# Kernel optimization log

Measured on AMD Instinct MI355X. Metric: run time of the kernel, lower is better.

The kernel has to match this reference:

```python
import jax, jax.numpy as jnp
from jax import lax
import numpy as np

B, T, IN, H = 512, 2048, 6, 32


def _gru_dir(x, Wih, bih, Whh, bhh, reverse):
    # x: [B, T, in]; PyTorch GRU gate order: r, z, n
    xp = jnp.einsum('bti,gi->btg', x, Wih) + bih  # [B, T, 3H] precompute input GEMM
    h0 = jnp.zeros((x.shape[0], Whh.shape[1]), x.dtype)

    def step(h, xt):
        gh = h @ Whh.T + bhh                      # [B, 3H]
        xr, xz, xn = jnp.split(xt, 3, axis=-1)
        hr, hz, hn = jnp.split(gh, 3, axis=-1)
        r = jax.nn.sigmoid(xr + hr)
        z = jax.nn.sigmoid(xz + hz)
        n = jnp.tanh(xn + r * hn)
        h_new = (1.0 - z) * n + z * h
        return h_new, h_new

    xs = jnp.swapaxes(xp, 0, 1)                   # [T, B, 3H]
    _, hs = lax.scan(step, h0, xs, reverse=reverse)  # ys aligned to time index
    return jnp.swapaxes(hs, 0, 1)                 # [B, T, H]


def setup_inputs() -> dict:
    key = jax.random.key(0)
    ks = jax.random.split(key, 32)
    s = 1.0 / np.sqrt(H)
    u = lambda k, shp: jax.random.uniform(k, shp, jnp.float32, -s, s)
    inp = {'x': jax.random.normal(ks[0], (B, T, IN), jnp.float32)}
    i = 1
    for l, din in ((0, IN), (1, 2 * H)):
        for d in ('f', 'b'):
            inp[f'Wih_l{l}_{d}'] = u(ks[i], (3 * H, din)); i += 1
            inp[f'Whh_l{l}_{d}'] = u(ks[i], (3 * H, H)); i += 1
            inp[f'bih_l{l}_{d}'] = u(ks[i], (3 * H,)); i += 1
            inp[f'bhh_l{l}_{d}'] = u(ks[i], (3 * H,)); i += 1
    inp['fc1_w'] = u(ks[i], (16, 2 * H)); i += 1
    inp['fc1_b'] = u(ks[i], (16,)); i += 1
    inp['fc2_w'] = u(ks[i], (1, 16)); i += 1
    inp['fc2_b'] = u(ks[i], (1,))
    return inp


def reference(x, Wih_l0_f, Whh_l0_f, bih_l0_f, bhh_l0_f,
              Wih_l0_b, Whh_l0_b, bih_l0_b, bhh_l0_b,
              Wih_l1_f, Whh_l1_f, bih_l1_f, bhh_l1_f,
              Wih_l1_b, Whh_l1_b, bih_l1_b, bhh_l1_b,
              fc1_w, fc1_b, fc2_w, fc2_b):
    # layer 0 bidirectional
    f0 = _gru_dir(x, Wih_l0_f, bih_l0_f, Whh_l0_f, bhh_l0_f, reverse=False)
    b0 = _gru_dir(x, Wih_l0_b, bih_l0_b, Whh_l0_b, bhh_l0_b, reverse=True)
    h0 = jnp.concatenate([f0, b0], axis=-1)       # [B, T, 2H]; inter-layer dropout: eval mode -> identity
    # layer 1 bidirectional
    f1 = _gru_dir(h0, Wih_l1_f, bih_l1_f, Whh_l1_f, bhh_l1_f, reverse=False)
    b1 = _gru_dir(h0, Wih_l1_b, bih_l1_b, Whh_l1_b, bhh_l1_b, reverse=True)
    out = jnp.concatenate([f1, b1], axis=-1)      # [B, T, 2H]
    pooled = jnp.mean(out, axis=1)                # [B, 2H]
    h = jax.nn.relu(pooled @ fc1_w.T + fc1_b)     # dropout: eval mode -> identity
    return h @ fc2_w.T + fc2_b                    # [B, 1]
```

## Files before the change

kernel.cpp:

```cpp
#include <hip/hip_runtime.h>

#define TB  512
#define TT  2048
#define HID 32

typedef _Float16 f16;
typedef float f32x2 __attribute__((ext_vector_type(2)));


#define PKFMA(ACC, A, B) \
  asm("v_pk_fma_f32 %0, %1, %2, %0" : "+v"(ACC) : "v"(A), "v"(B))

__device__ __forceinline__ float half_swap(float x, int half){
#if __has_builtin(__builtin_amdgcn_permlane32_swap)
  typedef unsigned uv2 __attribute__((ext_vector_type(2)));
  uv2 r = __builtin_amdgcn_permlane32_swap(__float_as_uint(x), __float_as_uint(x),
                                           false, false);
  return __uint_as_float(half ? r.x : r.y);
#else
  (void)half;
  return __shfl_xor(x, 32, 64);
#endif
}

__global__ __launch_bounds__(64,1)
void gru_l0(const float* __restrict__ x,
            const float* __restrict__ Wih_f, const float* __restrict__ Whh_f,
            const float* __restrict__ bih_f, const float* __restrict__ bhh_f,
            const float* __restrict__ Wih_b, const float* __restrict__ Whh_b,
            const float* __restrict__ bih_b, const float* __restrict__ bhh_b,
            f16* __restrict__ h0)
{
  const int job  = blockIdx.x;
  const int b    = job >> 1;
  const int dir  = job & 1;
  const int lane = threadIdx.x;
  const int j    = lane & 31;
  const int half = lane >> 5;

  const float* Wih = dir ? Wih_b : Wih_f;
  const float* Whh = dir ? Whh_b : Whh_f;
  const float* bih = dir ? bih_b : bih_f;
  const float* bhh = dir ? bhh_b : bhh_f;

  const int mrow = half * 32 + j;
  const int nrow = 64 + j;

  f32x2 wh_m2[16], wh_n2[16];
  f32x2 wi_m2[3],  wi_n2[3];
  {
    const float4* wm4 = (const float4*)(Whh + mrow*32);
#pragma unroll
    for (int q=0;q<8;q++){ float4 v=wm4[q];
      wh_m2[2*q]   = f32x2{v.x, v.y};
      wh_m2[2*q+1] = f32x2{v.z, v.w}; }
    const float4* wn4 = (const float4*)(Whh + nrow*32);
#pragma unroll
    for (int q=0;q<8;q++){ float4 v=wn4[q];
      wh_n2[2*q]   = f32x2{v.x, v.y};
      wh_n2[2*q+1] = f32x2{v.z, v.w}; }
#pragma unroll
    for (int i=0;i<3;i++){
      wi_m2[i] = f32x2{Wih[mrow*6+2*i], Wih[mrow*6+2*i+1]};
      wi_n2[i] = f32x2{Wih[nrow*6+2*i], Wih[nrow*6+2*i+1]};
    }
  }
  const float b_m   = bih[mrow] + bhh[mrow];
  const float b_ihn = bih[nrow];
  const float b_hhn = bhh[nrow];

  __shared__ __align__(16) float hlds[32];

  double hj = 0.;

  const long t0    = dir ? (TT-1) : 0;
  const long tstep = dir ? -1 : 1;
  const float* xrow = x + ((size_t)b*TT + t0)*6;
  const long  xinc = tstep*6;
  f16* hout = h0 + ((size_t)b*TT + t0)*64 + dir*32;
  const long hinc = tstep*64;

  f32x2 hp[16];
#pragma unroll
  for (int k=0;k<16;k++) hp[k]=f32x2{0.f,0.f};

#define L0_STEP(XV)                                                          \
  {                                                                          \
    f32x2 SX2 = f32x2{0.f,0.f}, SN2 = f32x2{0.f,0.f};                        \
    PKFMA(SX2, wi_m2[0], XV[0]); PKFMA(SN2, wi_n2[0], XV[0]);                \
    PKFMA(SX2, wi_m2[1], XV[1]); PKFMA(SN2, wi_n2[1], XV[1]);                \
    PKFMA(SX2, wi_m2[2], XV[2]); PKFMA(SN2, wi_n2[2], XV[2]);                \
    float sx  = SX2.x + SX2.y;                                               \
    float sxn = SN2.x + SN2.y;                                               \
    f32x2 A0=f32x2{0.f,0.f}, A1=f32x2{0.f,0.f};                              \
    f32x2 C0=f32x2{0.f,0.f}, C1=f32x2{0.f,0.f};                              \
    _Pragma("unroll")                                                        \
    for (int k=0;k<8;k++){                                                   \
      PKFMA(A0, wh_m2[2*k],   hp[2*k]);                                      \
      PKFMA(A1, wh_m2[2*k+1], hp[2*k+1]);                                    \
      PKFMA(C0, wh_n2[2*k],   hp[2*k]);                                      \
      PKFMA(C1, wh_n2[2*k+1], hp[2*k+1]);                                    \
    }                                                                        \
    float hm   = (A0.x+A0.y)+(A1.x+A1.y);                                    \
    float sn_h = (C0.x+C0.y)+(C1.x+C1.y);                                    \
    float vf   = hm + sx + b_m;                                              \
    float varg = half ? -vf : vf;                                            \
    float ef   = __builtin_amdgcn_exp2f(varg * -1.44269504088896341f);       \
    float gmf  = __builtin_amdgcn_rcpf(1.f + ef);                            \
    float wf   = half_swap(gmf, half);                                       \
    float xn = sxn + b_ihn;                                                  \
    float hn = sn_h + b_hhn;                                                 \
    float af = fmaf(gmf, hn, xn);                                            \
    float e2 = __builtin_amdgcn_exp2f(af * 2.88539008177792682f);            \
    float nnf= 1.f - 2.f*__builtin_amdgcn_rcpf(1.f + e2);                    \
    double hnew = fma((double)wf, (double)nnf - hj, hj);                     \
    hj = hnew;                                                               \
    if (lane < 32){ hlds[j] = (float)hnew; hout[j] = (f16)hnew; }            \
    hout += hinc;                                                            \
    {                                                                        \
      const float4* h4 = (const float4*)hlds;                                \
      _Pragma("unroll")                                                      \
      for (int q=0;q<8;q++){ float4 v=h4[q];                                 \
        hp[2*q]   = f32x2{v.x, v.y};                                         \
        hp[2*q+1] = f32x2{v.z, v.w}; }                                       \
    }                                                                        \
  }

  f32x2 xa[3], xb[3];
  {
    const float2* p=(const float2*)xrow;
    xa[0]=f32x2{p[0].x,p[0].y}; xa[1]=f32x2{p[1].x,p[1].y}; xa[2]=f32x2{p[2].x,p[2].y};
    const float2* q=(const float2*)(xrow + xinc);
    xb[0]=f32x2{q[0].x,q[0].y}; xb[1]=f32x2{q[1].x,q[1].y}; xb[2]=f32x2{q[2].x,q[2].y};
  }
  const float* xld = xrow + 2*xinc;

#pragma unroll 1
  for (int it=0; it<TT; it+=2){
    L0_STEP(xa)
    if (it+2 < TT){
      const float2* p=(const float2*)xld;
      xa[0]=f32x2{p[0].x,p[0].y}; xa[1]=f32x2{p[1].x,p[1].y}; xa[2]=f32x2{p[2].x,p[2].y};
      xld += xinc;
    }
    L0_STEP(xb)
    if (it+3 < TT){
      const float2* p=(const float2*)xld;
      xb[0]=f32x2{p[0].x,p[0].y}; xb[1]=f32x2{p[1].x,p[1].y}; xb[2]=f32x2{p[2].x,p[2].y};
      xld += xinc;
    }
  }
#undef L0_STEP
}

__global__ __launch_bounds__(128,2)
void gru_l1(const f16* __restrict__ h0,
            const float* __restrict__ Wih_f, const float* __restrict__ Whh_f,
            const float* __restrict__ bih_f, const float* __restrict__ bhh_f,
            const float* __restrict__ Wih_b, const float* __restrict__ Whh_b,
            const float* __restrict__ bih_b, const float* __restrict__ bhh_b,
            float* __restrict__ pooled)
{
  const int job  = blockIdx.x;
  const int b    = job >> 1;
  const int dir  = job & 1;
  const int tid  = threadIdx.x;
  const int wid  = tid >> 6;
  const int lane = tid & 63;
  const int j    = lane & 31;
  const int half = lane >> 5;

  const float* Wih = dir ? Wih_b : Wih_f;
  const float* Whh = dir ? Whh_b : Whh_f;
  const float* bih = dir ? bih_b : bih_f;
  const float* bhh = dir ? bhh_b : bhh_f;

  const int mrow = half * 32 + j;
  const int nrow = 64 + j;

  __shared__ __align__(16) float hlds[32];
  __shared__ __align__(16) float ring[8*64];
  __shared__ __align__(16) float fx[8][64];
  __shared__ __align__(16) float fn[8][64];

  const f16* h0b = h0 + (size_t)b*TT*64;
#define ROWF(LT) (h0b + (size_t)(dir ? (TT-1-(LT)) : (LT))*64)

  f32x2 wreg[48];
  float b_m=0.f, b_ihn=0.f, b_hhn=0.f;
  float pA=0.f, pB=0.f;

  if (wid == 1){
    const float4* wm4 = (const float4*)(Wih + mrow*64);
#pragma unroll
    for (int q=0;q<16;q++){ float4 v=wm4[q];
      wreg[2*q]   = f32x2{v.x,v.y};
      wreg[2*q+1] = f32x2{v.z,v.w}; }
    const float4* wn4 = (const float4*)(Wih + nrow*64 + half*32);
#pragma unroll
    for (int q=0;q<8;q++){ float4 v=wn4[q];
      wreg[32+2*q]   = f32x2{v.x,v.y};
      wreg[32+2*q+1] = f32x2{v.z,v.w}; }
  } else {
    const float4* hm4 = (const float4*)(Whh + mrow*32);
#pragma unroll
    for (int q=0;q<8;q++){ float4 v=hm4[q];
      wreg[2*q]   = f32x2{v.x,v.y};
      wreg[2*q+1] = f32x2{v.z,v.w}; }
    const float4* hn4 = (const float4*)(Whh + nrow*32 + half*16);
#pragma unroll
    for (int q=0;q<4;q++){ float4 v=hn4[q];
      wreg[16+2*q]   = f32x2{v.x,v.y};
      wreg[16+2*q+1] = f32x2{v.z,v.w}; }
    b_m   = bih[mrow] + bhh[mrow];
    b_ihn = bih[nrow];
    b_hhn = bhh[nrow];
    if (lane < 32) hlds[lane] = 0.f;
  }

#define PRODUCE(S)                                                           \
  {                                                                          \
    const int slot = (S)&7;                                                  \
    const float4* s4 = (const float4*)(ring + slot*64);                      \
    f32x2 M0=f32x2{0.f,0.f}, M1=f32x2{0.f,0.f};                              \
    f32x2 NA=f32x2{0.f,0.f}, NB=f32x2{0.f,0.f};                              \
    _Pragma("unroll")                                                        \
    for (int q=0;q<16;q++){ float4 v=s4[q];                                  \
      f32x2 lo = f32x2{v.x,v.y}, hi = f32x2{v.z,v.w};                        \
      PKFMA(M0, wreg[2*q],   lo);                                            \
      PKFMA(M1, wreg[2*q+1], hi);                                            \
      if (q<8){ PKFMA(NA, wreg[32+2*q],   lo);                               \
                PKFMA(NA, wreg[32+2*q+1], hi); }                             \
      else {    PKFMA(NB, wreg[32+2*(q-8)],   lo);                           \
                PKFMA(NB, wreg[32+2*(q-8)+1], hi); }                         \
    }                                                                        \
    fx[slot][lane] = (M0.x+M0.y)+(M1.x+M1.y);                                \
    fn[slot][lane] = half ? (NB.x+NB.y) : (NA.x+NA.y);                       \
  }

#define CORE(T)                                                              \
  {                                                                          \
    float sx = fx[(T)&7][lane];                                              \
    float sn = fn[(T)&7][lane];                                              \
    f32x2 A0=f32x2{0.f,0.f}, A1=f32x2{0.f,0.f};                              \
    {                                                                        \
      const float4* h4 = (const float4*)hlds;                                \
      _Pragma("unroll")                                                      \
      for (int q=0;q<8;q++){ float4 v=h4[q];                                 \
        PKFMA(A0, wreg[2*q],   (f32x2{v.x,v.y}));                            \
        PKFMA(A1, wreg[2*q+1], (f32x2{v.z,v.w}));                            \
      }                                                                      \
    }                                                                        \
    f32x2 C0=f32x2{0.f,0.f}, C1=f32x2{0.f,0.f};                              \
    {                                                                        \
      const float4* hx4 = (const float4*)(hlds + half*16);                   \
      _Pragma("unroll")                                                      \
      for (int q=0;q<4;q++){ float4 v=hx4[q];                                \
        PKFMA(C0, wreg[16+2*q],   (f32x2{v.x,v.y}));                         \
        PKFMA(C1, wreg[16+2*q+1], (f32x2{v.z,v.w}));                         \
      }                                                                      \
    }                                                                        \
    float hm   = (A0.x+A0.y)+(A1.x+A1.y);                                    \
    float sn_h = (C0.x+C0.y)+(C1.x+C1.y);                                    \
    float vf   = hm + sx + b_m;                                              \
    float varg = half ? -vf : vf;                                            \
    float ef   = __builtin_amdgcn_exp2f(varg * -1.44269504088896341f);       \
    float gmf  = __builtin_amdgcn_rcpf(1.f + ef);                            \
    float wf   = half_swap(gmf,  half);                                      \
    float xn_o = half_swap(sn,   half);                                      \
    float hn_o = half_swap(sn_h, half);                                      \
    float xn = sn + xn_o + b_ihn;                                            \
    float hn = sn_h + hn_o + b_hhn;                                          \
    float af = fmaf(gmf, hn, xn);                                            \
    float e2 = __builtin_amdgcn_exp2f(af * 2.88539008177792682f);            \
    float nnf= 1.f - 2.f*__builtin_amdgcn_rcpf(1.f + e2);                    \
    double hnew = fma((double)wf, (double)nnf - hj, hj);                     \
    hj = hnew;                                                               \
    psum += hnew;                                                            \
    if (lane < 32) hlds[j] = (float)hnew;                                    \
  }

  double hj = 0., psum = 0.;

  if (wid == 1){
    float pr[8];
#pragma unroll
    for (int k=0;k<8;k++){
      int lt = k; if (lt > TT-1) lt = TT-1;
      pr[k] = (float)ROWF(lt)[lane];
    }
#pragma unroll
    for (int k=0;k<6;k++) ring[k*64 + lane] = pr[k];
    pA = pr[6]; pB = pr[7];
    PRODUCE(0) PRODUCE(1) PRODUCE(2) PRODUCE(3)
  }

#pragma unroll 1
  for (int t=0; t<TT; t+=2){
    __syncthreads();
    if (wid == 0){
      CORE(t)
      CORE(t+1)
    } else {
      ring[((t+6)&7)*64 + lane] = pA;
      ring[((t+7)&7)*64 + lane] = pB;
      { int lt = t+8; if (lt > TT-1) lt = TT-1; pA = (float)ROWF(lt)[lane]; }
      { int lt = t+9; if (lt > TT-1) lt = TT-1; pB = (float)ROWF(lt)[lane]; }
      if (t+4 < TT) PRODUCE(t+4)
      if (t+5 < TT) PRODUCE(t+5)
    }
  }
#undef PRODUCE
#undef CORE
#undef ROWF

  if (wid == 0 && lane < 32)
    pooled[(size_t)b*64 + dir*32 + j] = (float)psum;
}

__global__ void fc_ep(const float* __restrict__ pooled,
                      const float* __restrict__ fc1w, const float* __restrict__ fc1b,
                      const float* __restrict__ fc2w, const float* __restrict__ fc2b,
                      float* __restrict__ out)
{
  int b = blockIdx.x*blockDim.x + threadIdx.x;
  if (b >= TB) return;
  float v[64];
  const float4* p4 = (const float4*)(pooled + (size_t)b*64);
#pragma unroll
  for (int q=0;q<16;q++){ float4 t=p4[q];
    v[4*q]  =t.x*(1.f/TT); v[4*q+1]=t.y*(1.f/TT);
    v[4*q+2]=t.z*(1.f/TT); v[4*q+3]=t.w*(1.f/TT); }
  float acc = fc2b[0];
#pragma unroll
  for (int g=0; g<16; g++){
    float s = fc1b[g];
    const float4* w4 = (const float4*)(fc1w + g*64);
#pragma unroll
    for (int q=0;q<16;q++){ float4 w=w4[q];
      s=fmaf(w.x,v[4*q],s);   s=fmaf(w.y,v[4*q+1],s);
      s=fmaf(w.z,v[4*q+2],s); s=fmaf(w.w,v[4*q+3],s); }
    s = fmaxf(s, 0.f);
    acc = fmaf(fc2w[g], s, acc);
  }
  out[b] = acc;
}

extern "C" void kernel_launch(void* const* d_in, const int* in_sizes, int n_in,
                              void* d_out, int out_size, void* d_ws, size_t ws_size,
                              hipStream_t stream)
{
  (void)in_sizes; (void)n_in; (void)out_size;

  const float* x     = (const float*)d_in[0];
  const float* Wih0f = (const float*)d_in[1];
  const float* Whh0f = (const float*)d_in[2];
  const float* bih0f = (const float*)d_in[3];
  const float* bhh0f = (const float*)d_in[4];
  const float* Wih0b = (const float*)d_in[5];
  const float* Whh0b = (const float*)d_in[6];
  const float* bih0b = (const float*)d_in[7];
  const float* bhh0b = (const float*)d_in[8];
  const float* Wih1f = (const float*)d_in[9];
  const float* Whh1f = (const float*)d_in[10];
  const float* bih1f = (const float*)d_in[11];
  const float* bhh1f = (const float*)d_in[12];
  const float* Wih1b = (const float*)d_in[13];
  const float* Whh1b = (const float*)d_in[14];
  const float* bih1b = (const float*)d_in[15];
  const float* bhh1b = (const float*)d_in[16];
  const float* fc1w  = (const float*)d_in[17];
  const float* fc1b  = (const float*)d_in[18];
  const float* fc2w  = (const float*)d_in[19];
  const float* fc2b  = (const float*)d_in[20];

  const size_t POOLED_BYTES = (size_t)TB * 64 * sizeof(float);
  const size_t PER_B        = (size_t)TT * 64 * sizeof(f16);
  float* pooled = (float*)d_ws;
  f16*   h0     = (f16*)((char*)d_ws + POOLED_BYTES);

  size_t avail = (ws_size > POOLED_BYTES) ? (ws_size - POOLED_BYTES) : 0;
  int Bc = (int)(avail / PER_B);
  if (Bc < 1)  Bc = 1;
  if (Bc > TB) Bc = TB;
  int nch = (TB + Bc - 1) / Bc;
  int Bce = (TB + nch - 1) / nch;

  for (int b0 = 0; b0 < TB; b0 += Bce) {
    int bc = (TB - b0 < Bce) ? (TB - b0) : Bce;
    hipLaunchKernelGGL(gru_l0, dim3(2*bc), dim3(64), 0, stream,
                       x + (size_t)b0*TT*6,
                       Wih0f,Whh0f,bih0f,bhh0f, Wih0b,Whh0b,bih0b,bhh0b, h0);
    hipLaunchKernelGGL(gru_l1, dim3(2*bc), dim3(128), 0, stream,
                       h0,
                       Wih1f,Whh1f,bih1f,bhh1f, Wih1b,Whh1b,bih1b,bhh1b,
                       pooled + (size_t)b0*64);
  }
  hipLaunchKernelGGL(fc_ep, dim3(2), dim3(256), 0, stream,
                     pooled, fc1w, fc1b, fc2w, fc2b, (float*)d_out);
}
```

Before: 2.096 ms.

## Broadcast hidden state via readlane instead of LDS round-trip in GRU recurrences

```diff
diff --git a/kernel.cpp b/kernel.cpp
--- a/kernel.cpp
+++ b/kernel.cpp
@@ -20,6 +20,14 @@
 #else
   (void)half;
   return __shfl_xor(x, 32, 64);
+#endif
+}
+
+__device__ __forceinline__ float rdlane(float x, int k){
+#if __has_builtin(__builtin_amdgcn_readlane)
+  return __uint_as_float(__builtin_amdgcn_readlane(__float_as_uint(x), k));
+#else
+  return __shfl(x, k, 64);
 #endif
 }
 
@@ -46,19 +54,17 @@
   const int mrow = half * 32 + j;
   const int nrow = 64 + j;
 
-  f32x2 wh_m2[16], wh_n2[16];
+  float wh_m[32], wh_n[32];
   f32x2 wi_m2[3],  wi_n2[3];
   {
     const float4* wm4 = (const float4*)(Whh + mrow*32);
 #pragma unroll
     for (int q=0;q<8;q++){ float4 v=wm4[q];
-      wh_m2[2*q]   = f32x2{v.x, v.y};
-      wh_m2[2*q+1] = f32x2{v.z, v.w}; }
+      wh_m[4*q]=v.x; wh_m[4*q+1]=v.y; wh_m[4*q+2]=v.z; wh_m[4*q+3]=v.w; }
     const float4* wn4 = (const float4*)(Whh + nrow*32);
 #pragma unroll
     for (int q=0;q<8;q++){ float4 v=wn4[q];
-      wh_n2[2*q]   = f32x2{v.x, v.y};
-      wh_n2[2*q+1] = f32x2{v.z, v.w}; }
+      wh_n[4*q]=v.x; wh_n[4*q+1]=v.y; wh_n[4*q+2]=v.z; wh_n[4*q+3]=v.w; }
 #pragma unroll
     for (int i=0;i<3;i++){
       wi_m2[i] = f32x2{Wih[mrow*6+2*i], Wih[mrow*6+2*i+1]};
@@ -69,20 +75,21 @@
   const float b_ihn = bih[nrow];
   const float b_hhn = bhh[nrow];
 
-  __shared__ __align__(16) float hlds[32];
-
+  float hs[32];
+#pragma unroll
+  for (int k=0;k<32;k++) hs[k]=0.f;
   double hj = 0.;
+
+  const float* xb_ = x + (size_t)b*TT*6;
+#define XROW(LT) (xb_ + (size_t)(dir ? (TT-1-(LT)) : (LT))*6)
+#define XLOAD(DST, LT) { const float2* p=(const float2*)XROW(LT);            \
+    DST[0]=f32x2{p[0].x,p[0].y}; DST[1]=f32x2{p[1].x,p[1].y};                \
+    DST[2]=f32x2{p[2].x,p[2].y}; }
 
   const long t0    = dir ? (TT-1) : 0;
   const long tstep = dir ? -1 : 1;
-  const float* xrow = x + ((size_t)b*TT + t0)*6;
-  const long  xinc = tstep*6;
   f16* hout = h0 + ((size_t)b*TT + t0)*64 + dir*32;
   const long hinc = tstep*64;
-
-  f32x2 hp[16];
-#pragma unroll
-  for (int k=0;k<16;k++) hp[k]=f32x2{0.f,0.f};
 
 #define L0_STEP(XV)                                                          \
   {                                                                          \
@@ -92,17 +99,20 @@
     PKFMA(SX2, wi_m2[2], XV[2]); PKFMA(SN2, wi_n2[2], XV[2]);                \
     float sx  = SX2.x + SX2.y;                                               \
     float sxn = SN2.x + SN2.y;                                               \
-    f32x2 A0=f32x2{0.f,0.f}, A1=f32x2{0.f,0.f};                              \
-    f32x2 C0=f32x2{0.f,0.f}, C1=f32x2{0.f,0.f};                              \
+    float a0=0.f,a1=0.f,a2=0.f,a3=0.f, c0=0.f,c1=0.f,c2=0.f,c3=0.f;          \
     _Pragma("unroll")                                                        \
     for (int k=0;k<8;k++){                                                   \
-      PKFMA(A0, wh_m2[2*k],   hp[2*k]);                                      \
-      PKFMA(A1, wh_m2[2*k+1], hp[2*k+1]);                                    \
-      PKFMA(C0, wh_n2[2*k],   hp[2*k]);                                      \
-      PKFMA(C1, wh_n2[2*k+1], hp[2*k+1]);                                    \
+      a0 = fmaf(wh_m[4*k+0], hs[4*k+0], a0);                                 \
+      a1 = fmaf(wh_m[4*k+1], hs[4*k+1], a1);                                 \
+      a2 = fmaf(wh_m[4*k+2], hs[4*k+2], a2);                                 \
+      a3 = fmaf(wh_m[4*k+3], hs[4*k+3], a3);                                 \
+      c0 = fmaf(wh_n[4*k+0], hs[4*k+0], c0);                                 \
+      c1 = fmaf(wh_n[4*k+1], hs[4*k+1], c1);                                 \
+      c2 = fmaf(wh_n[4*k+2], hs[4*k+2], c2);                                 \
+      c3 = fmaf(wh_n[4*k+3], hs[4*k+3], c3);                                 \
     }                                                                        \
-    float hm   = (A0.x+A0.y)+(A1.x+A1.y);                                    \
-    float sn_h = (C0.x+C0.y)+(C1.x+C1.y);                                    \
+    float hm   = (a0+a1)+(a2+a3);                                            \
+    float sn_h = (c0+c1)+(c2+c3);                                            \
     float vf   = hm + sx + b_m;                                              \
     float varg = half ? -vf : vf;                                            \
     float ef   = __builtin_amdgcn_exp2f(varg * -1.44269504088896341f);       \
@@ -115,42 +125,30 @@
     float nnf= 1.f - 2.f*__builtin_amdgcn_rcpf(1.f + e2);                    \
     double hnew = fma((double)wf, (double)nnf - hj, hj);                     \
     hj = hnew;                                                               \
-    if (lane < 32){ hlds[j] = (float)hnew; hout[j] = (f16)hnew; }            \
+    float hnf = (float)hnew;                                                 \
+    if (lane < 32) hout[j] = (f16)hnew;                                      \
     hout += hinc;                                                            \
-    {                                                                        \
-      const float4* h4 = (const float4*)hlds;                                \
-      _Pragma("unroll")                                                      \
-      for (int q=0;q<8;q++){ float4 v=h4[q];                                 \
-        hp[2*q]   = f32x2{v.x, v.y};                                         \
-        hp[2*q+1] = f32x2{v.z, v.w}; }                                       \
-    }                                                                        \
-  }
-
-  f32x2 xa[3], xb[3];
-  {
-    const float2* p=(const float2*)xrow;
-    xa[0]=f32x2{p[0].x,p[0].y}; xa[1]=f32x2{p[1].x,p[1].y}; xa[2]=f32x2{p[2].x,p[2].y};
-    const float2* q=(const float2*)(xrow + xinc);
-    xb[0]=f32x2{q[0].x,q[0].y}; xb[1]=f32x2{q[1].x,q[1].y}; xb[2]=f32x2{q[2].x,q[2].y};
-  }
-  const float* xld = xrow + 2*xinc;
+    _Pragma("unroll")                                                        \
+    for (int k=0;k<32;k++) hs[k] = rdlane(hnf, k);                           \
+  }
+
+  f32x2 xa[3], xb[3], xc[3], xd[3];
+  XLOAD(xa,0) XLOAD(xb,1) XLOAD(xc,2) XLOAD(xd,3)
 
 #pragma unroll 1
-  for (int it=0; it<TT; it+=2){
+  for (int it=0; it<TT; it+=4){
     L0_STEP(xa)
-    if (it+2 < TT){
-      const float2* p=(const float2*)xld;
-      xa[0]=f32x2{p[0].x,p[0].y}; xa[1]=f32x2{p[1].x,p[1].y}; xa[2]=f32x2{p[2].x,p[2].y};
-      xld += xinc;
-    }
+    { int lt=it+4; if(lt>TT-1) lt=TT-1; XLOAD(xa,lt) }
     L0_STEP(xb)
-    if (it+3 < TT){
-      const float2* p=(const float2*)xld;
-      xb[0]=f32x2{p[0].x,p[0].y}; xb[1]=f32x2{p[1].x,p[1].y}; xb[2]=f32x2{p[2].x,p[2].y};
-      xld += xinc;
-    }
+    { int lt=it+5; if(lt>TT-1) lt=TT-1; XLOAD(xb,lt) }
+    L0_STEP(xc)
+    { int lt=it+6; if(lt>TT-1) lt=TT-1; XLOAD(xc,lt) }
+    L0_STEP(xd)
+    { int lt=it+7; if(lt>TT-1) lt=TT-1; XLOAD(xd,lt) }
   }
 #undef L0_STEP
+#undef XLOAD
+#undef XROW
 }
 
 __global__ __launch_bounds__(128,2)
@@ -178,7 +176,6 @@
   const int mrow = half * 32 + j;
   const int nrow = 64 + j;
 
-  __shared__ __align__(16) float hlds[32];
   __shared__ __align__(16) float ring[8*64];
   __shared__ __align__(16) float fx[8][64];
   __shared__ __align__(16) float fn[8][64];
@@ -186,7 +183,7 @@
   const f16* h0b = h0 + (size_t)b*TT*64;
 #define ROWF(LT) (h0b + (size_t)(dir ? (TT-1-(LT)) : (LT))*64)
 
-  f32x2 wreg[48];
+  f32x2 wreg2[48];
   float b_m=0.f, b_ihn=0.f, b_hhn=0.f;
   float pA=0.f, pB=0.f;
 
@@ -194,93 +191,92 @@
     const float4* wm4 = (const float4*)(Wih + mrow*64);
 #pragma unroll
     for (int q=0;q<16;q++){ float4 v=wm4[q];
-      wreg[2*q]   = f32x2{v.x,v.y};
-      wreg[2*q+1] = f32x2{v.z,v.w}; }
+      wreg2[2*q]   = f32x2{v.x,v.y};
+      wreg2[2*q+1] = f32x2{v.z,v.w}; }
     const float4* wn4 = (const float4*)(Wih + nrow*64 + half*32);
 #pragma unroll
     for (int q=0;q<8;q++){ float4 v=wn4[q];
-      wreg[32+2*q]   = f32x2{v.x,v.y};
-      wreg[32+2*q+1] = f32x2{v.z,v.w}; }
+      wreg2[32+2*q]   = f32x2{v.x,v.y};
+      wreg2[32+2*q+1] = f32x2{v.z,v.w}; }
   } else {
     const float4* hm4 = (const float4*)(Whh + mrow*32);
 #pragma unroll
     for (int q=0;q<8;q++){ float4 v=hm4[q];
-      wreg[2*q]   = f32x2{v.x,v.y};
-      wreg[2*q+1] = f32x2{v.z,v.w}; }
-    const float4* hn4 = (const float4*)(Whh + nrow*32 + half*16);
-#pragma unroll
-    for (int q=0;q<4;q++){ float4 v=hn4[q];
-      wreg[16+2*q]   = f32x2{v.x,v.y};
-      wreg[16+2*q+1] = f32x2{v.z,v.w}; }
+      wreg2[2*q]   = f32x2{v.x,v.y};
+      wreg2[2*q+1] = f32x2{v.z,v.w}; }
+    const float4* hn4 = (const float4*)(Whh + nrow*32);
+#pragma unroll
+    for (int q=0;q<8;q++){ float4 v=hn4[q];
+      wreg2[16+2*q]   = f32x2{v.x,v.y};
+      wreg2[16+2*q+1] = f32x2{v.z,v.w}; }
     b_m   = bih[mrow] + bhh[mrow];
     b_ihn = bih[nrow];
     b_hhn = bhh[nrow];
-    if (lane < 32) hlds[lane] = 0.f;
-  }
+  }
+
+  float hs[32];
+#pragma unroll
+  for (int k=0;k<32;k++) hs[k]=0.f;
+  double hj = 0., psum = 0.;
 
 #define PRODUCE(S)                                                           \
   {                                                                          \
     const int slot = (S)&7;                                                  \
     const float4* s4 = (const float4*)(ring + slot*64);                      \
     f32x2 M0=f32x2{0.f,0.f}, M1=f32x2{0.f,0.f};                              \
-    f32x2 NA=f32x2{0.f,0.f}, NB=f32x2{0.f,0.f};                              \
     _Pragma("unroll")                                                        \
     for (int q=0;q<16;q++){ float4 v=s4[q];                                  \
-      f32x2 lo = f32x2{v.x,v.y}, hi = f32x2{v.z,v.w};                        \
-      PKFMA(M0, wreg[2*q],   lo);                                            \
-      PKFMA(M1, wreg[2*q+1], hi);                                            \
-      if (q<8){ PKFMA(NA, wreg[32+2*q],   lo);                               \
-                PKFMA(NA, wreg[32+2*q+1], hi); }                             \
-      else {    PKFMA(NB, wreg[32+2*(q-8)],   lo);                           \
-                PKFMA(NB, wreg[32+2*(q-8)+1], hi); }                         \
+      PKFMA(M0, wreg2[2*q],   (f32x2{v.x,v.y}));                             \
+      PKFMA(M1, wreg2[2*q+1], (f32x2{v.z,v.w}));                             \
     }                                                                        \
+    const float4* sn4 = (const float4*)(ring + slot*64) + half*8;            \
+    f32x2 N0=f32x2{0.f,0.f}, N1=f32x2{0.f,0.f};                              \
+    _Pragma("unroll")                                                        \
+    for (int q=0;q<8;q++){ float4 v=sn4[q];                                  \
+      PKFMA(N0, wreg2[32+2*q],   (f32x2{v.x,v.y}));                          \
+      PKFMA(N1, wreg2[32+2*q+1], (f32x2{v.z,v.w}));                          \
+    }                                                                        \
+    float own = (N0.x+N0.y)+(N1.x+N1.y);                                     \
+    float oth = half_swap(own, half);                                        \
     fx[slot][lane] = (M0.x+M0.y)+(M1.x+M1.y);                                \
-    fn[slot][lane] = half ? (NB.x+NB.y) : (NA.x+NA.y);                       \
+    fn[slot][lane] = own + oth;                                              \
   }
 
 #define CORE(T)                                                              \
   {                                                                          \
-    float sx = fx[(T)&7][lane];                                              \
-    float sn = fn[(T)&7][lane];                                              \
-    f32x2 A0=f32x2{0.f,0.f}, A1=f32x2{0.f,0.f};                              \
-    {                                                                        \
-      const float4* h4 = (const float4*)hlds;                                \
-      _Pragma("unroll")                                                      \
-      for (int q=0;q<8;q++){ float4 v=h4[q];                                 \
-        PKFMA(A0, wreg[2*q],   (f32x2{v.x,v.y}));                            \
-        PKFMA(A1, wreg[2*q+1], (f32x2{v.z,v.w}));                            \
-      }                                                                      \
+    float sx  = fx[(T)&7][lane];                                             \
+    float snt = fn[(T)&7][lane];                                             \
+    float a0=0.f,a1=0.f,a2=0.f,a3=0.f, c0=0.f,c1=0.f,c2=0.f,c3=0.f;          \
+    _Pragma("unroll")                                                        \
+    for (int q=0;q<8;q++){                                                   \
+      a0 = fmaf(wreg2[2*q].x,    hs[4*q+0], a0);                             \
+      a1 = fmaf(wreg2[2*q].y,    hs[4*q+1], a1);                             \
+      a2 = fmaf(wreg2[2*q+1].x,  hs[4*q+2], a2);                             \
+      a3 = fmaf(wreg2[2*q+1].y,  hs[4*q+3], a3);                             \
+      c0 = fmaf(wreg2[16+2*q].x, hs[4*q+0], c0);                             \
+      c1 = fmaf(wreg2[16+2*q].y, hs[4*q+1], c1);                             \
+      c2 = fmaf(wreg2[16+2*q+1].x, hs[4*q+2], c2);                           \
+      c3 = fmaf(wreg2[16+2*q+1].y, hs[4*q+3], c3);                           \
     }                                                                        \
-    f32x2 C0=f32x2{0.f,0.f}, C1=f32x2{0.f,0.f};                              \
-    {                                                                        \
-      const float4* hx4 = (const float4*)(hlds + half*16);                   \
-      _Pragma("unroll")                                                      \
-      for (int q=0;q<4;q++){ float4 v=hx4[q];                                \
-        PKFMA(C0, wreg[16+2*q],   (f32x2{v.x,v.y}));                         \
-        PKFMA(C1, wreg[16+2*q+1], (f32x2{v.z,v.w}));                         \
-      }                                                                      \
-    }                                                                        \
-    float hm   = (A0.x+A0.y)+(A1.x+A1.y);                                    \
-    float sn_h = (C0.x+C0.y)+(C1.x+C1.y);                                    \
+    float hm   = (a0+a1)+(a2+a3);                                            \
+    float sn_h = (c0+c1)+(c2+c3);                                            \
     float vf   = hm + sx + b_m;                                              \
     float varg = half ? -vf : vf;                                            \
     float ef   = __builtin_amdgcn_exp2f(varg * -1.44269504088896341f);       \
     float gmf  = __builtin_amdgcn_rcpf(1.f + ef);                            \
-    float wf   = half_swap(gmf,  half);                                      \
-    float xn_o = half_swap(sn,   half);                                      \
-    float hn_o = half_swap(sn_h, half);                                      \
-    float xn = sn + xn_o + b_ihn;                                            \
-    float hn = sn_h + hn_o + b_hhn;                                          \
+    float wf   = half_swap(gmf, half);                                       \
+    float xn = snt + b_ihn;                                                  \
+    float hn = sn_h + b_hhn;                                                 \
     float af = fmaf(gmf, hn, xn);                                            \
     float e2 = __builtin_amdgcn_exp2f(af * 2.88539008177792682f);            \
     float nnf= 1.f - 2.f*__builtin_amdgcn_rcpf(1.f + e2);                    \
     double hnew = fma((double)wf, (double)nnf - hj, hj);                     \
     hj = hnew;                                                               \
     psum += hnew;                                                            \
-    if (lane < 32) hlds[j] = (float)hnew;                                    \
-  }
-
-  double hj = 0., psum = 0.;
+    float hnf = (float)hnew;                                                 \
+    _Pragma("unroll")                                                        \
+    for (int k=0;k<32;k++) hs[k] = rdlane(hnf, k);                           \
+  }
 
   if (wid == 1){
     float pr[8];
```

Result: slower. 2.565 ms (+22.4%).
